# Performance work log

Measured on AMD Instinct MI355X. Metric: run time of the kernel, lower is better.

The kernel has to match this reference:

```python
import jax, jax.numpy as jnp
import numpy as np

MODEL_DIM = 256
HIST = 8
HID = 512
N_NEURONS = 64
IN_DIM = MODEL_DIM * (1 + HIST)  # 2304
BATCH = 32
FMIN, FMAX = 0.5, 40.0
TICK_INTERVAL = 0.1
LN_EPS = 1e-5


def setup_inputs() -> dict:
    key = jax.random.key(0)
    ks = jax.random.split(key, 8)
    def lin(k, shape, fan_in):
        return (jax.random.normal(k, shape, jnp.float32) / np.sqrt(fan_in)).astype(jnp.float32)
    return {
        "input_embedding": jax.random.normal(ks[0], (BATCH, MODEL_DIM), jnp.float32),
        "pre_activations": jax.random.normal(ks[1], (HIST, MODEL_DIM), jnp.float32),
        "Wp": lin(ks[2], (MODEL_DIM, MODEL_DIM), MODEL_DIM),
        "bp": jnp.zeros((MODEL_DIM,), jnp.float32),
        "W1": lin(ks[3], (N_NEURONS, IN_DIM, HID), IN_DIM),
        "b1": jnp.zeros((N_NEURONS, HID), jnp.float32),
        "W2": lin(ks[4], (N_NEURONS, HID, HID), HID),
        "b2": jnp.zeros((N_NEURONS, HID), jnp.float32),
        "W3": lin(ks[5], (N_NEURONS, HID, MODEL_DIM), HID),
        "b3": jnp.zeros((N_NEURONS, MODEL_DIM), jnp.float32),
        "gamma": jnp.ones((N_NEURONS, MODEL_DIM), jnp.float32),
        "beta": jnp.zeros((N_NEURONS, MODEL_DIM), jnp.float32),
        "tick": 7,
    }


def reference(input_embedding, pre_activations, Wp, bp, W1, b1, W2, b2, W3, b3, gamma, beta, tick):
    B = input_embedding.shape[0]
    # input projection, shared history broadcast across batch
    proj = input_embedding @ Wp + bp                               # (B, D)
    hist = jnp.broadcast_to(pre_activations.reshape(-1)[None, :], (B, HIST * MODEL_DIM))
    x = jnp.concatenate([proj, hist], axis=-1)                     # (B, IN_DIM)
    # all neurons' 3-layer MLPs as batched GEMMs (dropout in eval mode = identity)
    h = jax.nn.gelu(jnp.einsum('bi,nih->bnh', x, W1) + b1, approximate=False)
    h = jax.nn.gelu(jnp.einsum('bnh,nhg->bng', h, W2) + b2, approximate=False)
    y = jnp.einsum('bnh,nhd->bnd', h, W3) + b3                     # (B, N, D)
    # per-neuron LayerNorm over last dim
    mu = jnp.mean(y, axis=-1, keepdims=True)
    var = jnp.mean((y - mu) ** 2, axis=-1, keepdims=True)
    y = (y - mu) * jax.lax.rsqrt(var + LN_EPS) * gamma + beta
    # oscillator modulation: log-spaced freq, deterministic phase
    i = jnp.arange(N_NEURONS, dtype=jnp.float32)
    freq = FMIN * (FMAX / FMIN) ** (i / (N_NEURONS - 1))
    phase = jnp.mod(i * 2.3571, 2.0 * np.pi)
    t = tick * TICK_INTERVAL
    mod = 1.0 + 0.5 * jnp.sin(2.0 * np.pi * freq * t + phase)      # (N,)
    return y * mod[None, :, None]                                  # (B, N, D)
```

## Files before the change

kernel.cpp:

```cpp
#include <hip/hip_runtime.h>
#include <hip/hip_bf16.h>

#define MODEL_DIM 256
#define HIST 8
#define HID 512
#define NNEUR 64
#define IN_DIM 2304
#define BATCH 32

typedef float v4f __attribute__((ext_vector_type(4)));

__device__ __forceinline__ float geluf(float x) {
    return 0.5f * x * (1.0f + erff(x * 0.70710678118654752440f));
}
__device__ __forceinline__ float f4c(const float4& v, int j) {
    switch (j) { case 0: return v.x; case 1: return v.y; case 2: return v.z; default: return v.w; }
}
__device__ __forceinline__ float4 ntload4(const float* p) {
    v4f v = __builtin_nontemporal_load((const v4f*)p);
    return make_float4(v.x, v.y, v.z, v.w);
}
__device__ __forceinline__ unsigned short f2b(float f) {
    unsigned u = __float_as_uint(f);
    u += 0x7FFFu + ((u >> 16) & 1u);
    return (unsigned short)(u >> 16);
}
__device__ __forceinline__ float b2f(unsigned short h) {
    return __uint_as_float(((unsigned)h) << 16);
}
__device__ __forceinline__ ushort4 f4_to_b4(float4 v) {
    return make_ushort4(f2b(v.x), f2b(v.y), f2b(v.z), f2b(v.w));
}
__device__ __forceinline__ float4 b4_to_f4(ushort4 u) {
    return make_float4(b2f(u.x), b2f(u.y), b2f(u.z), b2f(u.w));
}

__global__ __launch_bounds__(256, 8) void k_hist(
        const float* __restrict__ pre, const float* __restrict__ W1,
        const float* __restrict__ emb, const float* __restrict__ Wp,
        const float* __restrict__ bp, float* __restrict__ proj,
        float* __restrict__ ph) {
    const int bid = blockIdx.x;
    const int t   = threadIdx.x;

    if (bid >= 2048) {
        const int b = bid - 2048;
        __shared__ float e[MODEL_DIM];
        e[t] = emb[b * MODEL_DIM + t];
        __syncthreads();
        float acc = bp[t];
        #pragma unroll 4
        for (int k = 0; k < MODEL_DIM; ++k)
            acc = fmaf(e[k], Wp[(size_t)k * MODEL_DIM + t], acc);
        proj[b * MODEL_DIM + t] = acc;
        return;
    }

    const int n  = bid >> 5;
    const int ks = (bid >> 1) & 15;
    const int ch = bid & 1;
    const int w  = t >> 6;
    const int l  = t & 63;
    const int k0 = ks * 128;
    const int cb = ch * 256;

    __shared__ float ps[128];
    __shared__ float red[4][256];
    if (t < 128) ps[t] = pre[k0 + t];
    __syncthreads();

    const float* W = W1 + (size_t)n * IN_DIM * HID
                        + (size_t)(MODEL_DIM + k0 + w * 32) * HID + cb + l * 4;
    const float* pw = ps + w * 32;

    float4 a = make_float4(0.f, 0.f, 0.f, 0.f);
    #pragma unroll 8
    for (int kk = 0; kk < 32; ++kk) {
        float4 wv = ntload4(W + (size_t)kk * HID);
        float s = pw[kk];
        a.x = fmaf(s, wv.x, a.x);
        a.y = fmaf(s, wv.y, a.y);
        a.z = fmaf(s, wv.z, a.z);
        a.w = fmaf(s, wv.w, a.w);
    }
    *((float4*)&red[w][l * 4]) = a;
    __syncthreads();

    if (t < 64) {
        const int c = t * 4;
        float4 r0 = *((const float4*)&red[0][c]);
        float4 r1 = *((const float4*)&red[1][c]);
        float4 r2 = *((const float4*)&red[2][c]);
        float4 r3 = *((const float4*)&red[3][c]);
        float4 o = make_float4(r0.x + r1.x + r2.x + r3.x,
                               r0.y + r1.y + r2.y + r3.y,
                               r0.z + r1.z + r2.z + r3.z,
                               r0.w + r1.w + r2.w + r3.w);
        *((float4*)(ph + ((size_t)ks * NNEUR + n) * HID + cb + c)) = o;
    }
}

__global__ __launch_bounds__(256, 4) void k_proj(
        const float* __restrict__ proj, const float* __restrict__ W1,
        const float* __restrict__ ph, float* __restrict__ phs,
        unsigned short* __restrict__ pp) {
    const int bid = blockIdx.x;
    const int t  = threadIdx.x;

    if (bid < 64) {
        const size_t slh = (size_t)NNEUR * HID;
        #pragma unroll
        for (int q = 0; q < 2; ++q) {
            const int c = t + q * 256;
            const float* h = ph + (size_t)bid * HID + c;
            float s = 0.0f;
            #pragma unroll
            for (int s5 = 0; s5 < 16; ++s5)
                s += h[(size_t)s5 * slh];
            phs[(size_t)bid * HID + c] = s;
        }
    }

    const int n  = bid >> 3;
    const int ct = (bid >> 2) & 1;
    const int ks = bid & 3;
    const int cg = t & 63;
    const int rg = t >> 6;
    const int col0 = ct * 256 + cg * 4;
    const int row0 = rg * 8;
    const int k0 = ks * 64;

    __shared__ float xs[BATCH][64];
    #pragma unroll
    for (int q = 0; q < 2; ++q) {
        int fi  = t + 256 * q;
        int row = fi >> 4;
        int c4v = fi & 15;
        *((float4*)&xs[row][c4v * 4]) =
            *((const float4*)(proj + (size_t)row * MODEL_DIM + k0 + c4v * 4));
    }
    __syncthreads();

    const float* W = W1 + (size_t)n * IN_DIM * HID + (size_t)k0 * HID + col0;

    float acc[8][4];
    #pragma unroll
    for (int i = 0; i < 8; ++i)
        #pragma unroll
        for (int j = 0; j < 4; ++j) acc[i][j] = 0.0f;

    for (int kg = 0; kg < 64; kg += 4) {
        float4 xv[8];
        #pragma unroll
        for (int i = 0; i < 8; ++i)
            xv[i] = *((const float4*)&xs[row0 + i][kg]);
        #pragma unroll
        for (int j = 0; j < 4; ++j) {
            float4 w = ntload4(W + (size_t)(kg + j) * HID);
            #pragma unroll
            for (int i = 0; i < 8; ++i) {
                float xvv = f4c(xv[i], j);
                acc[i][0] = fmaf(xvv, w.x, acc[i][0]);
                acc[i][1] = fmaf(xvv, w.y, acc[i][1]);
                acc[i][2] = fmaf(xvv, w.z, acc[i][2]);
                acc[i][3] = fmaf(xvv, w.w, acc[i][3]);
            }
        }
    }
    unsigned short* P = pp + (size_t)(ks * NNEUR + n) * BATCH * HID;
    #pragma unroll
    for (int i = 0; i < 8; ++i)
        *((ushort4*)(P + (size_t)(row0 + i) * HID + col0)) =
            f4_to_b4(make_float4(acc[i][0], acc[i][1], acc[i][2], acc[i][3]));
}

__global__ __launch_bounds__(256, 4) void k_layer2(
        const unsigned short* __restrict__ pp, const float* __restrict__ phs,
        const float* __restrict__ b1,
        const float* __restrict__ W2, unsigned short* __restrict__ p2) {
    const int bid = blockIdx.x;
    const int n  = bid >> 4;
    const int ct = (bid >> 3) & 1;
    const int ks = bid & 7;
    const int t  = threadIdx.x;
    const int cg = t & 63;
    const int rg = t >> 6;
    const int col0 = ct * 256 + cg * 4;
    const int row0 = rg * 8;
    const int k0 = ks * 64;

    const size_t slp = (size_t)NNEUR * BATCH * HID;

    __shared__ float xs[BATCH][64];
    #pragma unroll
    for (int q = 0; q < 2; ++q) {
        int fi  = t + 256 * q;
        int row = fi >> 4;
        int c4v = fi & 15;
        const unsigned short* a = pp + ((size_t)n * BATCH + row) * HID + k0 + c4v * 4;
        float4 s0 = b4_to_f4(*((const ushort4*)(a)));
        float4 s1 = b4_to_f4(*((const ushort4*)(a + slp)));
        float4 s2 = b4_to_f4(*((const ushort4*)(a + 2 * slp)));
        float4 s3 = b4_to_f4(*((const ushort4*)(a + 3 * slp)));
        float4 hs = *((const float4*)(phs + (size_t)n * HID + k0 + c4v * 4));
        float4 bb = *((const float4*)(b1 + (size_t)n * HID + k0 + c4v * 4));
        *((float4*)&xs[row][c4v * 4]) = make_float4(
            geluf(s0.x + s1.x + s2.x + s3.x + hs.x + bb.x),
            geluf(s0.y + s1.y + s2.y + s3.y + hs.y + bb.y),
            geluf(s0.z + s1.z + s2.z + s3.z + hs.z + bb.z),
            geluf(s0.w + s1.w + s2.w + s3.w + hs.w + bb.w));
    }
    __syncthreads();

    const float* W = W2 + (size_t)n * HID * HID + (size_t)k0 * HID + col0;

    float acc[8][4];
    #pragma unroll
    for (int i = 0; i < 8; ++i)
        #pragma unroll
        for (int j = 0; j < 4; ++j) acc[i][j] = 0.0f;

    for (int kg = 0; kg < 64; kg += 4) {
        float4 xv[8];
        #pragma unroll
        for (int i = 0; i < 8; ++i)
            xv[i] = *((const float4*)&xs[row0 + i][kg]);
        #pragma unroll
        for (int j = 0; j < 4; ++j) {
            float4 w = ntload4(W + (size_t)(kg + j) * HID);
            #pragma unroll
            for (int i = 0; i < 8; ++i) {
                float xvv = f4c(xv[i], j);
                acc[i][0] = fmaf(xvv, w.x, acc[i][0]);
                acc[i][1] = fmaf(xvv, w.y, acc[i][1]);
                acc[i][2] = fmaf(xvv, w.z, acc[i][2]);
                acc[i][3] = fmaf(xvv, w.w, acc[i][3]);
            }
        }
    }
    unsigned short* P = p2 + (size_t)(ks * NNEUR + n) * BATCH * HID;
    #pragma unroll
    for (int i = 0; i < 8; ++i)
        *((ushort4*)(P + (size_t)(row0 + i) * HID + col0)) =
            f4_to_b4(make_float4(acc[i][0], acc[i][1], acc[i][2], acc[i][3]));
}

__global__ __launch_bounds__(256, 4) void k_layer3(
        const unsigned short* __restrict__ p2, const float* __restrict__ b2,
        const float* __restrict__ W3, unsigned short* __restrict__ p3) {
    const int bid = blockIdx.x;
    const int n  = bid >> 4;
    const int ks = bid & 15;
    const int t  = threadIdx.x;
    const int cg = t & 63;
    const int rg = t >> 6;
    const int col0 = cg * 4;
    const int row0 = rg * 8;
    const int k0 = ks * 32;

    const size_t sl = (size_t)NNEUR * BATCH * HID;

    __shared__ float xs[BATCH][32];
    {
        int row = t >> 3;
        int c4v = t & 7;
        const unsigned short* a = p2 + ((size_t)n * BATCH + row) * HID + k0 + c4v * 4;
        float4 s0 = b4_to_f4(*((const ushort4*)(a)));
        float4 s1 = b4_to_f4(*((const ushort4*)(a + sl)));
        float4 s2 = b4_to_f4(*((const ushort4*)(a + 2 * sl)));
        float4 s3 = b4_to_f4(*((const ushort4*)(a + 3 * sl)));
        float4 s4 = b4_to_f4(*((const ushort4*)(a + 4 * sl)));
        float4 s5 = b4_to_f4(*((const ushort4*)(a + 5 * sl)));
        float4 s6 = b4_to_f4(*((const ushort4*)(a + 6 * sl)));
        float4 s7 = b4_to_f4(*((const ushort4*)(a + 7 * sl)));
        float4 bb = *((const float4*)(b2 + (size_t)n * HID + k0 + c4v * 4));
        *((float4*)&xs[row][c4v * 4]) = make_float4(
            geluf(s0.x+s1.x+s2.x+s3.x+s4.x+s5.x+s6.x+s7.x + bb.x),
            geluf(s0.y+s1.y+s2.y+s3.y+s4.y+s5.y+s6.y+s7.y + bb.y),
            geluf(s0.z+s1.z+s2.z+s3.z+s4.z+s5.z+s6.z+s7.z + bb.z),
            geluf(s0.w+s1.w+s2.w+s3.w+s4.w+s5.w+s6.w+s7.w + bb.w));
    }
    __syncthreads();

    const float* W = W3 + (size_t)n * HID * MODEL_DIM + (size_t)k0 * MODEL_DIM + col0;

    float acc[8][4];
    #pragma unroll
    for (int i = 0; i < 8; ++i)
        #pragma unroll
        for (int j = 0; j < 4; ++j) acc[i][j] = 0.0f;

    for (int kg = 0; kg < 32; kg += 4) {
        float4 xv[8];
        #pragma unroll
        for (int i = 0; i < 8; ++i)
            xv[i] = *((const float4*)&xs[row0 + i][kg]);
        #pragma unroll
        for (int j = 0; j < 4; ++j) {
            float4 w = ntload4(W + (size_t)(kg + j) * MODEL_DIM);
            #pragma unroll
            for (int i = 0; i < 8; ++i) {
                float xvv = f4c(xv[i], j);
                acc[i][0] = fmaf(xvv, w.x, acc[i][0]);
                acc[i][1] = fmaf(xvv, w.y, acc[i][1]);
                acc[i][2] = fmaf(xvv, w.z, acc[i][2]);
                acc[i][3] = fmaf(xvv, w.w, acc[i][3]);
            }
        }
    }
    unsigned short* P = p3 + (size_t)(ks * NNEUR + n) * BATCH * MODEL_DIM;
    #pragma unroll
    for (int i = 0; i < 8; ++i)
        *((ushort4*)(P + (size_t)(row0 + i) * MODEL_DIM + col0)) =
            f4_to_b4(make_float4(acc[i][0], acc[i][1], acc[i][2], acc[i][3]));
}

__global__ __launch_bounds__(256) void k_final(
        const unsigned short* __restrict__ p3, const float* __restrict__ b3,
        const float* __restrict__ gamma, const float* __restrict__ beta,
        const int* __restrict__ tick, float* __restrict__ out) {
    const int n  = blockIdx.x >> 3;
    const int bq = blockIdx.x & 7;
    const int t  = threadIdx.x;
    const int w  = t >> 6;
    const int lane = t & 63;
    const int b  = bq * 4 + w;

    const size_t par0 = (size_t)n * MODEL_DIM;
    const size_t rowoff = ((size_t)n * BATCH + b) * MODEL_DIM;
    const size_t sl = (size_t)NNEUR * BATCH * MODEL_DIM;

    float y[4];
    #pragma unroll
    for (int j = 0; j < 4; ++j) {
        int d = lane + 64 * j;
        float v = b3[par0 + d];
        #pragma unroll
        for (int s = 0; s < 16; ++s)
            v += b2f(p3[s * sl + rowoff + d]);
        y[j] = v;
    }
    float s = y[0] + y[1] + y[2] + y[3];
    #pragma unroll
    for (int off = 32; off > 0; off >>= 1) s += __shfl_xor(s, off);
    float mu = s * (1.0f / 256.0f);
    float q = 0.0f;
    #pragma unroll
    for (int j = 0; j < 4; ++j) { float d0 = y[j] - mu; q = fmaf(d0, d0, q); }
    #pragma unroll
    for (int off = 32; off > 0; off >>= 1) q += __shfl_xor(q, off);
    float inv = rsqrtf(q * (1.0f / 256.0f) + 1e-5f);

    const double TWO_PI = 6.283185307179586476925287;
    double freq  = 0.5 * pow(80.0, (double)n * (1.0 / 63.0));
    double phase = fmod((double)n * 2.3571, TWO_PI);
    double tt    = (double)(*tick) * 0.1;
    float mod = (float)(1.0 + 0.5 * sin(TWO_PI * freq * tt + phase));

    #pragma unroll
    for (int j = 0; j < 4; ++j) {
        int d = lane + 64 * j;
        float o = (y[j] - mu) * inv * gamma[par0 + d] + beta[par0 + d];
        o *= mod;
        out[((size_t)b * NNEUR + n) * MODEL_DIM + d] = o;
    }
}

extern "C" void kernel_launch(void* const* d_in, const int* in_sizes, int n_in,
                              void* d_out, int out_size, void* d_ws, size_t ws_size,
                              hipStream_t stream) {
    const float* emb  = (const float*)d_in[0];
    const float* pre  = (const float*)d_in[1];
    const float* Wp   = (const float*)d_in[2];
    const float* bp   = (const float*)d_in[3];
    const float* W1   = (const float*)d_in[4];
    const float* b1   = (const float*)d_in[5];
    const float* W2   = (const float*)d_in[6];
    const float* b2   = (const float*)d_in[7];
    const float* W3   = (const float*)d_in[8];
    const float* b3   = (const float*)d_in[9];
    const float* gam  = (const float*)d_in[10];
    const float* bet  = (const float*)d_in[11];
    const int* tick   = (const int*)d_in[12];

    float* ws = (float*)d_ws;
    float* proj = ws;
    float* ph  = proj + 8192;
    float* phs = ph + 524288;
    unsigned short* pp = (unsigned short*)(phs + 32768);
    unsigned short* p2 = pp + 4194304;
    unsigned short* p3 = p2 + 8388608;
    float* out = (float*)d_out;

    k_hist   <<<2080, 256, 0, stream>>>(pre, W1, emb, Wp, bp, proj, ph);
    k_proj   <<<512,  256, 0, stream>>>(proj, W1, ph, phs, pp);
    k_layer2 <<<1024, 256, 0, stream>>>(pp, phs, b1, W2, p2);
    k_layer3 <<<1024, 256, 0, stream>>>(p2, b2, W3, p3);
    k_final  <<<512,  256, 0, stream>>>(p3, b3, gam, bet, tick, out);
}
```

Measured before the change: 137.1 us.

## Stream W1 history rows through LDS with async global_load_lds double buffering

```diff
diff --git a/kernel.cpp b/kernel.cpp
--- a/kernel.cpp
+++ b/kernel.cpp
@@ -9,6 +9,8 @@
 #define BATCH 32
 
 typedef float v4f __attribute__((ext_vector_type(4)));
+typedef const __attribute__((address_space(1))) void* gptr_t;
+typedef __attribute__((address_space(3))) void* lptr_t;
 
 __device__ __forceinline__ float geluf(float x) {
     return 0.5f * x * (1.0f + erff(x * 0.70710678118654752440f));
@@ -19,6 +21,9 @@
 __device__ __forceinline__ float4 ntload4(const float* p) {
     v4f v = __builtin_nontemporal_load((const v4f*)p);
     return make_float4(v.x, v.y, v.z, v.w);
+}
+__device__ __forceinline__ void gll16(const float* g, float* l) {
+    __builtin_amdgcn_global_load_lds((gptr_t)g, (lptr_t)l, 16, 0, 0);
 }
 __device__ __forceinline__ unsigned short f2b(float f) {
     unsigned u = __float_as_uint(f);
@@ -35,13 +40,17 @@
     return make_float4(b2f(u.x), b2f(u.y), b2f(u.z), b2f(u.w));
 }
 
-__global__ __launch_bounds__(256, 8) void k_hist(
+__global__ __launch_bounds__(256, 4) void k_hist(
         const float* __restrict__ pre, const float* __restrict__ W1,
         const float* __restrict__ emb, const float* __restrict__ Wp,
         const float* __restrict__ bp, float* __restrict__ proj,
         float* __restrict__ ph) {
     const int bid = blockIdx.x;
     const int t   = threadIdx.x;
+
+    __shared__ float ps[128];
+    __shared__ float red[4][256];
+    __shared__ float wbuf[4][2][4][256];
 
     if (bid >= 2048) {
         const int b = bid - 2048;
@@ -64,25 +73,45 @@
     const int k0 = ks * 128;
     const int cb = ch * 256;
 
-    __shared__ float ps[128];
-    __shared__ float red[4][256];
     if (t < 128) ps[t] = pre[k0 + t];
     __syncthreads();
 
-    const float* W = W1 + (size_t)n * IN_DIM * HID
-                        + (size_t)(MODEL_DIM + k0 + w * 32) * HID + cb + l * 4;
+    const float* Wb = W1 + (size_t)n * IN_DIM * HID
+                         + (size_t)(MODEL_DIM + k0 + w * 32) * HID + cb;
+    const float* gl = Wb + l * 4;
     const float* pw = ps + w * 32;
+    float* buf0 = &wbuf[w][0][0][0];
+    float* buf1 = &wbuf[w][1][0][0];
+
+    #pragma unroll
+    for (int r = 0; r < 4; ++r)
+        gll16(gl + (size_t)r * HID, buf0 + r * 256);
 
     float4 a = make_float4(0.f, 0.f, 0.f, 0.f);
-    #pragma unroll 8
-    for (int kk = 0; kk < 32; ++kk) {
-        float4 wv = ntload4(W + (size_t)kk * HID);
-        float s = pw[kk];
-        a.x = fmaf(s, wv.x, a.x);
-        a.y = fmaf(s, wv.y, a.y);
-        a.z = fmaf(s, wv.z, a.z);
-        a.w = fmaf(s, wv.w, a.w);
-    }
+    #pragma unroll
+    for (int bi = 0; bi < 8; ++bi) {
+        float* cur = (bi & 1) ? buf1 : buf0;
+        float* nxt = (bi & 1) ? buf0 : buf1;
+        if (bi < 7) {
+            #pragma unroll
+            for (int r = 0; r < 4; ++r)
+                gll16(gl + (size_t)((bi + 1) * 4 + r) * HID, nxt + r * 256);
+            asm volatile("s_waitcnt vmcnt(4)" ::: "memory");
+        } else {
+            asm volatile("s_waitcnt vmcnt(0)" ::: "memory");
+        }
+        __builtin_amdgcn_sched_barrier(0);
+        #pragma unroll
+        for (int r = 0; r < 4; ++r) {
+            float s = pw[bi * 4 + r];
+            float4 wv = *((const float4*)(cur + r * 256 + l * 4));
+            a.x = fmaf(s, wv.x, a.x);
+            a.y = fmaf(s, wv.y, a.y);
+            a.z = fmaf(s, wv.z, a.z);
+            a.w = fmaf(s, wv.w, a.w);
+        }
+    }
+
     *((float4*)&red[w][l * 4]) = a;
     __syncthreads();
 
```

After: 136.1 us. No clear change (-0.7%).

## Stream W1 history rows through LDS with async global_load_lds triple buffering

Applied to the files above, without the earlier changes.

```diff
diff --git a/kernel.cpp b/kernel.cpp
--- a/kernel.cpp
+++ b/kernel.cpp
@@ -9,6 +9,8 @@
 #define BATCH 32
 
 typedef float v4f __attribute__((ext_vector_type(4)));
+typedef const __attribute__((address_space(1))) void* gptr_t;
+typedef __attribute__((address_space(3))) void* lptr_t;
 
 __device__ __forceinline__ float geluf(float x) {
     return 0.5f * x * (1.0f + erff(x * 0.70710678118654752440f));
@@ -19,6 +21,9 @@
 __device__ __forceinline__ float4 ntload4(const float* p) {
     v4f v = __builtin_nontemporal_load((const v4f*)p);
     return make_float4(v.x, v.y, v.z, v.w);
+}
+__device__ __forceinline__ void gll16(const float* g, float* l) {
+    __builtin_amdgcn_global_load_lds((gptr_t)g, (lptr_t)l, 16, 0, 0);
 }
 __device__ __forceinline__ unsigned short f2b(float f) {
     unsigned u = __float_as_uint(f);
@@ -42,6 +47,10 @@
         float* __restrict__ ph) {
     const int bid = blockIdx.x;
     const int t   = threadIdx.x;
+
+    __shared__ float ps[128];
+    __shared__ float red[4][256];
+    __shared__ float wbuf[4][3][256];
 
     if (bid >= 2048) {
         const int b = bid - 2048;
@@ -64,25 +73,41 @@
     const int k0 = ks * 128;
     const int cb = ch * 256;
 
-    __shared__ float ps[128];
-    __shared__ float red[4][256];
     if (t < 128) ps[t] = pre[k0 + t];
     __syncthreads();
 
-    const float* W = W1 + (size_t)n * IN_DIM * HID
-                        + (size_t)(MODEL_DIM + k0 + w * 32) * HID + cb + l * 4;
+    const float* Wb = W1 + (size_t)n * IN_DIM * HID
+                         + (size_t)(MODEL_DIM + k0 + w * 32) * HID + cb;
+    const float* gl = Wb + l * 4;
     const float* pw = ps + w * 32;
+    float* b0 = &wbuf[w][0][0];
+    float* b1 = &wbuf[w][1][0];
+    float* b2 = &wbuf[w][2][0];
+
+    gll16(gl,                   b0);
+    gll16(gl + (size_t)1 * HID, b1);
+    gll16(gl + (size_t)2 * HID, b2);
 
     float4 a = make_float4(0.f, 0.f, 0.f, 0.f);
-    #pragma unroll 8
-    for (int kk = 0; kk < 32; ++kk) {
-        float4 wv = ntload4(W + (size_t)kk * HID);
-        float s = pw[kk];
-        a.x = fmaf(s, wv.x, a.x);
-        a.y = fmaf(s, wv.y, a.y);
-        a.z = fmaf(s, wv.z, a.z);
-        a.w = fmaf(s, wv.w, a.w);
-    }
+    #pragma unroll
+    for (int bi = 0; bi < 32; ++bi) {
+        float* cur = (bi % 3 == 0) ? b0 : ((bi % 3 == 1) ? b1 : b2);
+        if (bi <= 29)      asm volatile("s_waitcnt vmcnt(2)" ::: "memory");
+        else if (bi == 30) asm volatile("s_waitcnt vmcnt(1)" ::: "memory");
+        else               asm volatile("s_waitcnt vmcnt(0)" ::: "memory");
+        __builtin_amdgcn_sched_barrier(0);
+        {
+            float s = pw[bi];
+            float4 wv = *((const float4*)(cur + l * 4));
+            a.x = fmaf(s, wv.x, a.x);
+            a.y = fmaf(s, wv.y, a.y);
+            a.z = fmaf(s, wv.z, a.z);
+            a.w = fmaf(s, wv.w, a.w);
+        }
+        if (bi + 3 < 32)
+            gll16(gl + (size_t)(bi + 3) * HID, cur);
+    }
+
     *((float4*)&red[w][l * 4]) = a;
     __syncthreads();
 
```

Result: no change. 135.1 us (-1.5%).
